# Performance work log

Measured on AMD Instinct MI355X. Metric: run time of the kernel, lower is better.

Reference implementation:

```python
import jax, jax.numpy as jnp
import numpy as np

N_RAYS = 8192
N_SAMPLES = 64
N_IMPORTANCE = 64
N_UP_ITERS = 4
NEAR, FAR = 0.5, 4.0
S_FINAL = 64.0


def sdf_net(pts, W1, b1, W2, b2, W3, b3):
    # pts: [..., 3] -> sdf [...]
    h = jax.nn.relu(pts @ W1 + b1)
    h = jax.nn.relu(h @ W2 + b2)
    return (h @ W3 + b3)[..., 0]


def radiance_net(pts, dirs, R1, r1, R2, r2):
    x = jnp.concatenate([pts, dirs], axis=-1)  # [..., 6]
    h = jax.nn.relu(x @ R1 + r1)
    return jax.nn.sigmoid(h @ R2 + r2)  # [..., 3]


def cdf_Phi_s(x, s):
    return jax.nn.sigmoid(x * s)


def alpha_to_w(alpha):
    # w_i = alpha_i * prod_{j<i} (1 - alpha_j)
    shifted = jnp.concatenate([jnp.ones_like(alpha[..., :1]), 1.0 - alpha + 1e-10], axis=-1)
    return alpha * jnp.cumprod(shifted, axis=-1)[..., :-1]


def sample_pdf(bins, weights, N):
    # bins: [R, M], weights: [R, M-1]; deterministic inverse-CDF sampling
    weights = weights + 1e-5
    pdf = weights / jnp.sum(weights, axis=-1, keepdims=True)
    cdf = jnp.cumsum(pdf, axis=-1)
    cdf = jnp.concatenate([jnp.zeros_like(cdf[..., :1]), cdf], axis=-1)  # [R, M]
    u = jnp.broadcast_to(jnp.linspace(0.0, 1.0, N, dtype=bins.dtype), cdf.shape[:-1] + (N,))
    inds = jax.vmap(lambda c, uu: jnp.searchsorted(c, uu, side='right'))(cdf, u)
    M = cdf.shape[-1]
    below = jnp.clip(inds - 1, 0, M - 1)
    above = jnp.clip(inds, 0, M - 1)
    cdf_b = jnp.take_along_axis(cdf, below, -1)
    cdf_a = jnp.take_along_axis(cdf, above, -1)
    bins_b = jnp.take_along_axis(bins, below, -1)
    bins_a = jnp.take_along_axis(bins, above, -1)
    denom = cdf_a - cdf_b
    denom = jnp.where(denom < 1e-5, jnp.ones_like(denom), denom)
    t = (u - cdf_b) / denom
    return bins_b + t * (bins_a - bins_b)


def _forward(rays_o, rays_d, W1, b1, W2, b2, W3, b3, R1, r1, R2, r2, s_val):
    rays_o = rays_o.reshape(-1, 3).astype(jnp.float32)
    rays_d = rays_d.reshape(-1, 3).astype(jnp.float32)
    rays_d = rays_d / jnp.linalg.norm(rays_d, axis=-1, keepdims=True)

    _t = jnp.linspace(0.0, 1.0, N_SAMPLES, dtype=jnp.float32)
    near = jnp.full((rays_o.shape[0], 1), NEAR, dtype=jnp.float32)
    far = jnp.full((rays_o.shape[0], 1), FAR, dtype=jnp.float32)
    d = near * (1.0 - _t) + far * _t  # [R, N_SAMPLES]

    sdf_fn = lambda p: sdf_net(p, W1, b1, W2, b2, W3, b3)

    # --- hierarchical upsampling (no_grad in original; stop_gradient at end) ---
    sdf = sdf_fn(rays_o[:, None, :] + d[..., None] * rays_d[:, None, :])
    for i in range(N_UP_ITERS):
        prev_sdf, next_sdf = sdf[..., :-1], sdf[..., 1:]
        prev_z, next_z = d[..., :-1], d[..., 1:]
        mid_sdf = 0.5 * (prev_sdf + next_sdf)
        dot_val = (next_sdf - prev_sdf) / (next_z - prev_z + 1e-5)
        prev_dot = jnp.concatenate([jnp.zeros_like(dot_val[..., :1]), dot_val[..., :-1]], axis=-1)
        dot_val = jnp.clip(jnp.minimum(prev_dot, dot_val), -10.0, 0.0)
        dist = next_z - prev_z
        prev_esti = mid_sdf - dot_val * dist * 0.5
        next_esti = mid_sdf + dot_val * dist * 0.5
        s_i = 64.0 * (2.0 ** i)
        prev_cdf = cdf_Phi_s(prev_esti, s_i)
        next_cdf = cdf_Phi_s(next_esti, s_i)
        alpha = (prev_cdf - next_cdf + 1e-5) / (prev_cdf + 1e-5)
        w = alpha_to_w(alpha)
        d_fine = sample_pdf(d, w, N_IMPORTANCE // N_UP_ITERS)
        d = jnp.concatenate([d, d_fine], axis=-1)
        sdf_fine = sdf_fn(rays_o[:, None, :] + d_fine[..., None] * rays_d[:, None, :])
        sdf = jnp.concatenate([sdf, sdf_fine], axis=-1)
        idx = jnp.argsort(d, axis=-1)
        d = jnp.take_along_axis(d, idx, axis=-1)
        sdf = jnp.take_along_axis(sdf, idx, axis=-1)
    d_all = jax.lax.stop_gradient(d)  # [R, 128]

    # --- final compositing ---
    pts = rays_o[:, None, :] + d_all[..., None] * rays_d[:, None, :]  # [R, 128, 3]
    d_mid = 0.5 * (d_all[..., 1:] + d_all[..., :-1])  # [R, 127]
    pts_mid = rays_o[:, None, :] + d_mid[..., None] * rays_d[:, None, :]

    sdf_final = sdf_fn(pts)  # [R, 128]
    s = s_val[0] * S_FINAL
    cdf = cdf_Phi_s(sdf_final, s)
    opacity_alpha = jnp.clip((cdf[..., :-1] - cdf[..., 1:] + 1e-5) / (cdf[..., :-1] + 1e-5), 0.0, 1.0)  # [R, 127]

    view_dirs = jnp.broadcast_to(rays_d[:, None, :], pts_mid.shape)
    radiances = radiance_net(pts_mid, view_dirs, R1, r1, R2, r2)  # [R, 127, 3]

    vis_w = alpha_to_w(opacity_alpha)  # [R, 127]
    rgb_map = jnp.sum(vis_w[..., None] * radiances, axis=-2)  # [R, 3]
    depth_map = jnp.sum(vis_w * d_mid, axis=-1)  # [R]
    acc_map = jnp.sum(vis_w, axis=-1)  # [R]
    return jnp.concatenate([rgb_map, depth_map[..., None], acc_map[..., None]], axis=-1)  # [R, 5]


def setup_inputs() -> dict:
    key = jax.random.key(0)
    ks = jax.random.split(key, 16)
    W = 128
    sc = 0.3
    return {
        'rays_o': jax.random.normal(ks[0], (N_RAYS, 3), jnp.float32),
        'rays_d': jax.random.normal(ks[1], (N_RAYS, 3), jnp.float32),
        'W1': sc * jax.random.normal(ks[2], (3, W), jnp.float32),
        'b1': sc * jax.random.normal(ks[3], (W,), jnp.float32),
        'W2': sc / np.sqrt(W) * jax.random.normal(ks[4], (W, W), jnp.float32),
        'b2': sc * jax.random.normal(ks[5], (W,), jnp.float32),
        'W3': sc / np.sqrt(W) * jax.random.normal(ks[6], (W, 1), jnp.float32),
        'b3': sc * jax.random.normal(ks[7], (1,), jnp.float32),
        'R1': sc * jax.random.normal(ks[8], (6, W), jnp.float32),
        'r1': sc * jax.random.normal(ks[9], (W,), jnp.float32),
        'R2': sc / np.sqrt(W) * jax.random.normal(ks[10], (W, 3), jnp.float32),
        'r2': sc * jax.random.normal(ks[11], (3,), jnp.float32),
        's_val': jnp.ones((1,), jnp.float32),
    }


def reference(rays_o, rays_d, W1, b1, W2, b2, W3, b3, R1, r1, R2, r2, s_val):
    return _forward(rays_o, rays_d, W1, b1, W2, b2, W3, b3, R1, r1, R2, r2, s_val)
```

## Files before the change

### kernel.cpp

```cpp
#include <hip/hip_runtime.h>
#include <math.h>

#define NRAYS 8192
#define RPB 8
#define AS 136

typedef _Float16 half8 __attribute__((ext_vector_type(8)));
typedef float floatx4 __attribute__((ext_vector_type(4)));

__device__ __forceinline__ float sigm(float x){ return 1.0f/(1.0f + __expf(-x)); }

__device__ __forceinline__ void wsync(){
  __builtin_amdgcn_wave_barrier();
  __builtin_amdgcn_s_waitcnt(0xc07f);
  __builtin_amdgcn_wave_barrier();
}

__launch_bounds__(512, 4)
__global__ void neus_render_kernel(
    const float* __restrict__ rays_o, const float* __restrict__ rays_d,
    const float* __restrict__ W1, const float* __restrict__ b1,
    const float* __restrict__ W2, const float* __restrict__ b2,
    const float* __restrict__ W3, const float* __restrict__ b3,
    const float* __restrict__ R1, const float* __restrict__ r1,
    const float* __restrict__ R2, const float* __restrict__ r2,
    const float* __restrict__ s_val, float* __restrict__ out)
{
  __shared__ __align__(16) _Float16 W2f[2048*8];
  __shared__ __align__(16) _Float16 R2f[256*8];
  __shared__ __align__(16) _Float16 Ah[RPB][16*AS];
  __shared__ __align__(16) float sDm[RPB][128];
  __shared__ __align__(16) float sSm[RPB][128];
  __shared__ __align__(16) float fDs[RPB][16];
  __shared__ __align__(16) float fSs[RPB][16];
  __shared__ float b2f[128], w3f[128];

  const int t = threadIdx.x;

  #pragma unroll
  for (int r=0;r<4;r++){
    int row = t + r*512;
    int i = row>>8, kt=(row>>6)&3, lr=row&63;
    int q = lr>>4, n = i*16 + (lr&15);
    half8 v;
    #pragma unroll
    for (int j=0;j<8;j++) v[j] = (_Float16)W2[(kt*32+q*8+j)*128 + n];
    *(half8*)&W2f[row*8] = v;
  }
  if (t < 256){
    int kt=t>>6, lr=t&63, q=lr>>4, col=lr&15;
    half8 v;
    #pragma unroll
    for (int j=0;j<8;j++){
      int k = kt*32+q*8+j;
      v[j] = (col<3) ? (_Float16)R2[k*3+col] : (_Float16)0.0f;
    }
    *(half8*)&R2f[t*8] = v;
  }
  if (t < 128){ b2f[t]=b2[t]; w3f[t]=W3[t]; }
  __syncthreads();

  const int wv = t>>6, l = t&63, l15 = t&15, q4 = (t>>4)&3;
  const int ray = blockIdx.x*RPB + wv;

  float ro0 = rays_o[ray*3+0], ro1 = rays_o[ray*3+1], ro2 = rays_o[ray*3+2];
  float rx  = rays_d[ray*3+0], ry  = rays_d[ray*3+1], rz  = rays_d[ray*3+2];
  float nrm = sqrtf(rx*rx + ry*ry + rz*rz);
  float rd0 = rx/nrm, rd1 = ry/nrm, rd2 = rz/nrm;
  float sfin = s_val[0] * 64.0f;
  float b3v = b3[0];
  float r2lane = (l15==0) ? r2[0] : (l15==1) ? r2[1] : (l15==2) ? r2[2] : 0.0f;

  float u10, v10, u11, v11, uR0, vR0, uR1, vR1;
  {
    int k=l;
    float a=W1[k], b=W1[128+k], c=W1[256+k];
    u10 = rd0*a+rd1*b+rd2*c; v10 = ro0*a+ro1*b+ro2*c + b1[k];
    float p=R1[k], qq=R1[128+k], s=R1[256+k], d=R1[384+k], e=R1[512+k], f=R1[640+k];
    uR0 = rd0*p+rd1*qq+rd2*s;
    vR0 = ro0*p+ro1*qq+ro2*s + rd0*d+rd1*e+rd2*f + r1[k];
  }
  {
    int k=64+l;
    float a=W1[k], b=W1[128+k], c=W1[256+k];
    u11 = rd0*a+rd1*b+rd2*c; v11 = ro0*a+ro1*b+ro2*c + b1[k];
    float p=R1[k], qq=R1[128+k], s=R1[256+k], d=R1[384+k], e=R1[512+k], f=R1[640+k];
    uR1 = rd0*p+rd1*qq+rd2*s;
    vR1 = ro0*p+ro1*qq+ro2*s + rd0*d+rd1*e+rd2*f + r1[k];
  }

  _Float16* Ahw = &Ah[wv][0];
  float* sD = &sDm[wv][0];
  float* sS = &sSm[wv][0];

  auto eval16 = [&](const float* dptr, float* dstptr){
    const float4* dp4 = (const float4*)dptr;
    float4 dva = dp4[0], dvb = dp4[1], dvc = dp4[2], dvd = dp4[3];
    float dvals[16] = {dva.x,dva.y,dva.z,dva.w, dvb.x,dvb.y,dvb.z,dvb.w,
                       dvc.x,dvc.y,dvc.z,dvc.w, dvd.x,dvd.y,dvd.z,dvd.w};
    #pragma unroll
    for (int m=0;m<16;m++){
      float h0 = fmaxf(fmaf(dvals[m], u10, v10), 0.0f);
      float h1 = fmaxf(fmaf(dvals[m], u11, v11), 0.0f);
      Ahw[m*AS + l]      = (_Float16)h0;
      Ahw[m*AS + 64 + l] = (_Float16)h1;
    }
    wsync();
    half8 A[4];
    #pragma unroll
    for (int kt=0;kt<4;kt++)
      A[kt] = *(const half8*)&Ahw[l15*AS + kt*32 + q4*8];
    floatx4 acc[8];
    #pragma unroll
    for (int i=0;i<8;i++) acc[i] = (floatx4){0.f,0.f,0.f,0.f};
    #pragma unroll
    for (int i=0;i<8;i++){
      #pragma unroll
      for (int kt=0;kt<4;kt++){
        half8 B = *(const half8*)&W2f[((i*4+kt)*64 + l)*8];
        acc[i] = __builtin_amdgcn_mfma_f32_16x16x32_f16(A[kt], B, acc[i], 0,0,0);
      }
    }
    float p0=0.f,p1=0.f,p2=0.f,p3=0.f;
    #pragma unroll
    for (int i=0;i<8;i++){
      float bb = b2f[i*16+l15], ww = w3f[i*16+l15];
      p0 += fmaxf(acc[i][0]+bb,0.0f)*ww;
      p1 += fmaxf(acc[i][1]+bb,0.0f)*ww;
      p2 += fmaxf(acc[i][2]+bb,0.0f)*ww;
      p3 += fmaxf(acc[i][3]+bb,0.0f)*ww;
    }
    #pragma unroll
    for (int off=1; off<16; off<<=1){
      p0 += __shfl_xor(p0, off, 64);
      p1 += __shfl_xor(p1, off, 64);
      p2 += __shfl_xor(p2, off, 64);
      p3 += __shfl_xor(p3, off, 64);
    }
    if (l15==0){
      floatx4 o = {p0+b3v, p1+b3v, p2+b3v, p3+b3v};
      *((floatx4*)&dstptr[q4*4]) = o;
    }
    wsync();
  };

  {
    float tt = (float)l / 63.0f;
    sD[l] = 0.5f*(1.0f-tt) + 4.0f*tt;
  }
  wsync();
  for (int c=0;c<4;c++) eval16(&sD[c*16], &sS[c*16]);

  for (int it=0; it<4; it++){
    const int n = 64 + 16*it;
    const int m = n-1;
    const float s_i = 64.0f * (float)(1<<it);

    float dc0 = sD[l],  sc0 = sS[l];
    float dn0 = sD[l+1], snn0 = sS[l+1];
    int lp0 = (l==0)?0:(l-1);
    float dp0 = sD[lp0], sp0 = sS[lp0];
    int i1 = 64+l;
    float dc1 = sD[i1 & 127], sc1 = sS[i1 & 127];
    int i1n = (i1+1) & 127;
    float dn1 = sD[i1n], snn1 = sS[i1n];
    float dp1 = sD[(i1-1) & 127], sp1 = sS[(i1-1) & 127];

    auto alpha_at = [&](float dp, float dc, float dn, float sp, float sc, float sn,
                        bool hasprev)->float{
      float mid = 0.5f*(sc+sn);
      float dv = (sn-sc)/(dn-dc+1e-5f);
      float pdv = hasprev ? (sc-sp)/(dc-dp+1e-5f) : 0.0f;
      float d2 = fminf(fminf(pdv,dv), 0.0f); d2 = fmaxf(d2,-10.0f);
      float dist = dn-dc;
      float pe = mid - d2*dist*0.5f, ne = mid + d2*dist*0.5f;
      float pc = sigm(pe*s_i), nc = sigm(ne*s_i);
      return (pc-nc+1e-5f)/(pc+1e-5f);
    };
    bool va0 = (l < m), va1 = (i1 < m);
    float a0 = va0 ? alpha_at(dp0,dc0,dn0,sp0,sc0,snn0, l>0)  : 0.0f;
    float a1 = va1 ? alpha_at(dp1,dc1,dn1,sp1,sc1,snn1, true) : 0.0f;

    float g0 = va0 ? (1.0f-a0+1e-10f) : 1.0f;
    float g1 = va1 ? (1.0f-a1+1e-10f) : 1.0f;
    #pragma unroll
    for (int off=1; off<64; off<<=1){ float y=__shfl_up(g0,off,64); if (l>=off) g0*=y; }
    float gtot0 = __shfl(g0, 63, 64);
    #pragma unroll
    for (int off=1; off<64; off<<=1){ float y=__shfl_up(g1,off,64); if (l>=off) g1*=y; }
    g1 *= gtot0;
    float T0 = __shfl_up(g0, 1, 64); if (l==0) T0 = 1.0f;
    float T1 = __shfl_up(g1, 1, 64); if (l==0) T1 = gtot0;

    float w0 = va0 ? (a0*T0 + 1e-5f) : 0.0f;
    float w1 = va1 ? (a1*T1 + 1e-5f) : 0.0f;
    #pragma unroll
    for (int off=1; off<64; off<<=1){ float y=__shfl_up(w0,off,64); if (l>=off) w0+=y; }
    float wtot0 = __shfl(w0, 63, 64);
    #pragma unroll
    for (int off=1; off<64; off<<=1){ float y=__shfl_up(w1,off,64); if (l>=off) w1+=y; }
    w1 += wtot0;
    float S = (m-1 < 64) ? __shfl(w0, m-1, 64) : __shfl(w1, m-65, 64);

    float csp0 = __shfl_up(w0, 1, 64);
    float cdf0 = (l==0) ? 0.0f : csp0/S;
    float csp1 = __shfl_up(w1, 1, 64);
    float c63  = __shfl(w0, 63, 64);
    float cdf1r = ((l==0) ? c63 : csp1)/S;
    float cdf1m = (i1 < n) ? cdf1r : 2.0f;

    int ind = 0;
    #pragma unroll
    for (int q=0;q<16;q++){
      float u = (float)q/15.0f;
      unsigned long long bq0 = __ballot(cdf0 <= u);
      unsigned long long bq1 = __ballot(cdf1m <= u);
      int c = __popcll(bq0) + __popcll(bq1);
      if (l==q) ind = c;
    }
    {
      float u = (float)l15/15.0f;
      int below = ind-1; if (below<0) below=0; if (below>n-1) below=n-1;
      int above = ind;   if (above>n-1) above=n-1;
      float cb = (below<64) ? __shfl(cdf0, below, 64) : __shfl(cdf1r, below-64, 64);
      float ca = (above<64) ? __shfl(cdf0, above, 64) : __shfl(cdf1r, above-64, 64);
      float bb = sD[below], ba = sD[above];
      float den = ca - cb; if (den < 1e-5f) den = 1.0f;
      float tt = (u - cb)/den;
      float fdnew = bb + tt*(ba-bb);
      if (l < 16) fDs[wv][l] = fdnew;
    }
    wsync();

    eval16(&fDs[wv][0], &fSs[wv][0]);

    {
      const float4* fp4 = (const float4*)&fDs[wv][0];
      float4 fa = fp4[0], fb = fp4[1], fc = fp4[2], fd = fp4[3];
      float fq[16] = {fa.x,fa.y,fa.z,fa.w, fb.x,fb.y,fb.z,fb.w,
                      fc.x,fc.y,fc.z,fc.w, fd.x,fd.y,fd.z,fd.w};
      float fdv = fDs[wv][l15];
      float fsv = fSs[wv][l15];
      bool v1 = (i1 < n);
      int rold0 = l, rold1 = i1;
      #pragma unroll
      for (int q=0;q<16;q++){
        rold0 += (fq[q] < dc0) ? 1 : 0;
        rold1 += (fq[q] < dc1) ? 1 : 0;
      }
      int rf = 0;
      #pragma unroll
      for (int q=0;q<16;q++){
        unsigned long long bq0 = __ballot(dc0 <= fq[q]);
        unsigned long long bq1 = __ballot(v1 && (dc1 <= fq[q]));
        int c = q + __popcll(bq0) + __popcll(bq1);
        if (l==q) rf = c;
      }
      wsync();
      sD[rold0] = dc0; sS[rold0] = sc0;
      if (v1){ sD[rold1] = dc1; sS[rold1] = sc1; }
      if (l < 16){ sD[rf] = fdv; sS[rf] = fsv; }
      wsync();
    }
  }

  float dm0, dm1, vw0, vw1;
  {
    float d0 = sD[l],  d1 = sD[64+l];
    float s0 = sS[l],  s1 = sS[64+l];
    float dn0 = sD[l+1], sn0 = sS[l+1];
    int i1n = (65+l) & 127;
    float dn1 = sD[i1n], sn1 = sS[i1n];
    bool v1a = (l < 63);
    float cf0 = sigm(s0*sfin), cfn0 = sigm(sn0*sfin);
    float a0 = (cf0-cfn0+1e-5f)/(cf0+1e-5f);
    a0 = fminf(fmaxf(a0,0.0f),1.0f);
    float cf1 = sigm(s1*sfin), cfn1 = sigm(sn1*sfin);
    float a1 = (cf1-cfn1+1e-5f)/(cf1+1e-5f);
    a1 = v1a ? fminf(fmaxf(a1,0.0f),1.0f) : 0.0f;
    dm0 = 0.5f*(d0+dn0);
    dm1 = v1a ? 0.5f*(d1+dn1) : 0.0f;

    float g0 = 1.0f-a0+1e-10f;
    float g1 = v1a ? (1.0f-a1+1e-10f) : 1.0f;
    #pragma unroll
    for (int off=1; off<64; off<<=1){ float y=__shfl_up(g0,off,64); if (l>=off) g0*=y; }
    float gtot0 = __shfl(g0, 63, 64);
    #pragma unroll
    for (int off=1; off<64; off<<=1){ float y=__shfl_up(g1,off,64); if (l>=off) g1*=y; }
    g1 *= gtot0;
    float T0 = __shfl_up(g0, 1, 64); if (l==0) T0 = 1.0f;
    float T1 = __shfl_up(g1, 1, 64); if (l==0) T1 = gtot0;
    vw0 = a0*T0;
    vw1 = a1*T1;
    wsync();
    sD[l] = dm0; sD[64+l] = dm1;
    sS[l] = vw0; sS[64+l] = vw1;
    wsync();
  }

  half8 RB[4];
  #pragma unroll
  for (int kt=0;kt<4;kt++) RB[kt] = *(const half8*)&R2f[(kt*64+l)*8];
  float rgb = 0.0f;
  for (int g=0; g<8; g++){
    const float4* dp4 = (const float4*)&sDm[wv][g*16];
    float4 dva = dp4[0], dvb = dp4[1], dvc = dp4[2], dvd = dp4[3];
    float dvals[16] = {dva.x,dva.y,dva.z,dva.w, dvb.x,dvb.y,dvb.z,dvb.w,
                       dvc.x,dvc.y,dvc.z,dvc.w, dvd.x,dvd.y,dvd.z,dvd.w};
    #pragma unroll
    for (int m=0;m<16;m++){
      float h0 = fmaxf(fmaf(dvals[m], uR0, vR0), 0.0f);
      float h1 = fmaxf(fmaf(dvals[m], uR1, vR1), 0.0f);
      Ahw[m*AS + l]      = (_Float16)h0;
      Ahw[m*AS + 64 + l] = (_Float16)h1;
    }
    wsync();
    half8 A[4];
    #pragma unroll
    for (int kt=0;kt<4;kt++)
      A[kt] = *(const half8*)&Ahw[l15*AS + kt*32 + q4*8];
    floatx4 racc = (floatx4){0.f,0.f,0.f,0.f};
    #pragma unroll
    for (int kt=0;kt<4;kt++)
      racc = __builtin_amdgcn_mfma_f32_16x16x32_f16(A[kt], RB[kt], racc, 0,0,0);
    #pragma unroll
    for (int r=0;r<4;r++){
      int pt = g*16 + q4*4 + r;
      float w = sS[pt];
      rgb += w * sigm(racc[r] + r2lane);
    }
    wsync();
  }

  float v3 = dm0*vw0 + dm1*vw1;
  float v4 = vw0 + vw1;
  #pragma unroll
  for (int off=32; off>=1; off>>=1){
    v3 += __shfl_xor(v3, off, 64);
    v4 += __shfl_xor(v4, off, 64);
  }
  rgb += __shfl_xor(rgb, 16, 64);
  rgb += __shfl_xor(rgb, 32, 64);
  if (l < 3)  out[ray*5 + l] = rgb;
  if (l == 3) out[ray*5 + 3] = v3;
  if (l == 4) out[ray*5 + 4] = v4;
}

extern "C" void kernel_launch(void* const* d_in, const int* in_sizes, int n_in,
                              void* d_out, int out_size, void* d_ws, size_t ws_size,
                              hipStream_t stream) {
  const float* rays_o = (const float*)d_in[0];
  const float* rays_d = (const float*)d_in[1];
  const float* W1 = (const float*)d_in[2];
  const float* b1 = (const float*)d_in[3];
  const float* W2 = (const float*)d_in[4];
  const float* b2 = (const float*)d_in[5];
  const float* W3 = (const float*)d_in[6];
  const float* b3 = (const float*)d_in[7];
  const float* R1 = (const float*)d_in[8];
  const float* r1 = (const float*)d_in[9];
  const float* R2 = (const float*)d_in[10];
  const float* r2 = (const float*)d_in[11];
  const float* sv = (const float*)d_in[12];
  float* out = (float*)d_out;
  neus_render_kernel<<<NRAYS/RPB, 512, 0, stream>>>(
      rays_o, rays_d, W1, b1, W2, b2, W3, b3, R1, r1, R2, r2, sv, out);
}
```

Baseline: 188.5 us.

## Split SDF hidden activations into fp16 hi/lo pairs for extra MFMA precision

```diff
diff --git a/kernel.cpp b/kernel.cpp
--- a/kernel.cpp
+++ b/kernel.cpp
@@ -6,6 +6,7 @@
 #define AS 136
 
 typedef _Float16 half8 __attribute__((ext_vector_type(8)));
+typedef _Float16 half2v __attribute__((ext_vector_type(2)));
 typedef float floatx4 __attribute__((ext_vector_type(4)));
 
 __device__ __forceinline__ float sigm(float x){ return 1.0f/(1.0f + __expf(-x)); }
@@ -15,6 +16,82 @@
   __builtin_amdgcn_s_waitcnt(0xc07f);
   __builtin_amdgcn_wave_barrier();
 }
+
+#define EVAL16(dptr_, dstptr_) do { \
+  const float* dp_ = (dptr_); \
+  _Pragma("unroll") \
+  for (int mq=0;mq<4;mq++){ \
+    float4 dv4 = ((const float4*)dp_)[mq]; \
+    float h0_, h1_; \
+    h0_ = fmaxf(fmaf(dv4.x, u10, v10), 0.0f); h1_ = fmaxf(fmaf(dv4.x, u11, v11), 0.0f); \
+    *(half2v*)&Ahw[(mq*4+0)*AS + 2*l] = (half2v){(_Float16)h0_, (_Float16)h1_}; \
+    h0_ = fmaxf(fmaf(dv4.y, u10, v10), 0.0f); h1_ = fmaxf(fmaf(dv4.y, u11, v11), 0.0f); \
+    *(half2v*)&Ahw[(mq*4+1)*AS + 2*l] = (half2v){(_Float16)h0_, (_Float16)h1_}; \
+    h0_ = fmaxf(fmaf(dv4.z, u10, v10), 0.0f); h1_ = fmaxf(fmaf(dv4.z, u11, v11), 0.0f); \
+    *(half2v*)&Ahw[(mq*4+2)*AS + 2*l] = (half2v){(_Float16)h0_, (_Float16)h1_}; \
+    h0_ = fmaxf(fmaf(dv4.w, u10, v10), 0.0f); h1_ = fmaxf(fmaf(dv4.w, u11, v11), 0.0f); \
+    *(half2v*)&Ahw[(mq*4+3)*AS + 2*l] = (half2v){(_Float16)h0_, (_Float16)h1_}; \
+  } \
+  wsync(); \
+  half8 Ahi0 = *(const half8*)&Ahw[l15*AS +   0 + q4*8]; \
+  half8 Ahi1 = *(const half8*)&Ahw[l15*AS +  32 + q4*8]; \
+  half8 Ahi2 = *(const half8*)&Ahw[l15*AS +  64 + q4*8]; \
+  half8 Ahi3 = *(const half8*)&Ahw[l15*AS +  96 + q4*8]; \
+  wsync();    \
+  _Pragma("unroll") \
+  for (int mq=0;mq<4;mq++){ \
+    float4 dv4 = ((const float4*)dp_)[mq]; \
+    float h0_, h1_; _Float16 hh0_, hh1_; \
+    h0_ = fmaxf(fmaf(dv4.x, u10, v10), 0.0f); h1_ = fmaxf(fmaf(dv4.x, u11, v11), 0.0f); \
+    hh0_=(_Float16)h0_; hh1_=(_Float16)h1_; \
+    *(half2v*)&Ahw[(mq*4+0)*AS + 2*l] = (half2v){(_Float16)(h0_-(float)hh0_), (_Float16)(h1_-(float)hh1_)}; \
+    h0_ = fmaxf(fmaf(dv4.y, u10, v10), 0.0f); h1_ = fmaxf(fmaf(dv4.y, u11, v11), 0.0f); \
+    hh0_=(_Float16)h0_; hh1_=(_Float16)h1_; \
+    *(half2v*)&Ahw[(mq*4+1)*AS + 2*l] = (half2v){(_Float16)(h0_-(float)hh0_), (_Float16)(h1_-(float)hh1_)}; \
+    h0_ = fmaxf(fmaf(dv4.z, u10, v10), 0.0f); h1_ = fmaxf(fmaf(dv4.z, u11, v11), 0.0f); \
+    hh0_=(_Float16)h0_; hh1_=(_Float16)h1_; \
+    *(half2v*)&Ahw[(mq*4+2)*AS + 2*l] = (half2v){(_Float16)(h0_-(float)hh0_), (_Float16)(h1_-(float)hh1_)}; \
+    h0_ = fmaxf(fmaf(dv4.w, u10, v10), 0.0f); h1_ = fmaxf(fmaf(dv4.w, u11, v11), 0.0f); \
+    hh0_=(_Float16)h0_; hh1_=(_Float16)h1_; \
+    *(half2v*)&Ahw[(mq*4+3)*AS + 2*l] = (half2v){(_Float16)(h0_-(float)hh0_), (_Float16)(h1_-(float)hh1_)}; \
+  } \
+  wsync(); \
+  floatx4 acc[8]; \
+  _Pragma("unroll") \
+  for (int i=0;i<8;i++) acc[i] = (floatx4){0.f,0.f,0.f,0.f}; \
+  _Pragma("unroll") \
+  for (int kt=0;kt<4;kt++){ \
+    half8 Ahi_ = (kt==0)?Ahi0:(kt==1)?Ahi1:(kt==2)?Ahi2:Ahi3; \
+    half8 Alo_ = *(const half8*)&Ahw[l15*AS + kt*32 + q4*8]; \
+    _Pragma("unroll") \
+    for (int i=0;i<8;i++){ \
+      half8 B_ = *(const half8*)&W2f[((i*4+kt)*64 + l)*8]; \
+      acc[i] = __builtin_amdgcn_mfma_f32_16x16x32_f16(Ahi_, B_, acc[i], 0,0,0); \
+      acc[i] = __builtin_amdgcn_mfma_f32_16x16x32_f16(Alo_, B_, acc[i], 0,0,0); \
+    } \
+  } \
+  float p0=0.f,p1=0.f,p2=0.f,p3=0.f; \
+  _Pragma("unroll") \
+  for (int i=0;i<8;i++){ \
+    float bb = b2f[i*16+l15], ww = w3f[i*16+l15]; \
+    p0 += fmaxf(acc[i][0]+bb,0.0f)*ww; \
+    p1 += fmaxf(acc[i][1]+bb,0.0f)*ww; \
+    p2 += fmaxf(acc[i][2]+bb,0.0f)*ww; \
+    p3 += fmaxf(acc[i][3]+bb,0.0f)*ww; \
+  } \
+  _Pragma("unroll") \
+  for (int off=1; off<16; off<<=1){ \
+    p0 += __shfl_xor(p0, off, 64); \
+    p1 += __shfl_xor(p1, off, 64); \
+    p2 += __shfl_xor(p2, off, 64); \
+    p3 += __shfl_xor(p3, off, 64); \
+  } \
+  if (l15==0){ \
+    floatx4 o_ = {p0+b3v, p1+b3v, p2+b3v, p3+b3v}; \
+    *((floatx4*)&(dstptr_)[q4*4]) = o_; \
+  } \
+  wsync(); \
+} while(0)
 
 __launch_bounds__(512, 4)
 __global__ void neus_render_kernel(
@@ -62,94 +139,32 @@
 
   const int wv = t>>6, l = t&63, l15 = t&15, q4 = (t>>4)&3;
   const int ray = blockIdx.x*RPB + wv;
-
-  float ro0 = rays_o[ray*3+0], ro1 = rays_o[ray*3+1], ro2 = rays_o[ray*3+2];
-  float rx  = rays_d[ray*3+0], ry  = rays_d[ray*3+1], rz  = rays_d[ray*3+2];
-  float nrm = sqrtf(rx*rx + ry*ry + rz*rz);
-  float rd0 = rx/nrm, rd1 = ry/nrm, rd2 = rz/nrm;
-  float sfin = s_val[0] * 64.0f;
   float b3v = b3[0];
-  float r2lane = (l15==0) ? r2[0] : (l15==1) ? r2[1] : (l15==2) ? r2[2] : 0.0f;
-
-  float u10, v10, u11, v11, uR0, vR0, uR1, vR1;
+
+  float u10, v10, u11, v11;
   {
-    int k=l;
+    float ro0 = rays_o[ray*3+0], ro1 = rays_o[ray*3+1], ro2 = rays_o[ray*3+2];
+    float rx  = rays_d[ray*3+0], ry  = rays_d[ray*3+1], rz  = rays_d[ray*3+2];
+    float nrm = sqrtf(rx*rx + ry*ry + rz*rz);
+    float rd0 = rx/nrm, rd1 = ry/nrm, rd2 = rz/nrm;
+    int k=2*l;
     float a=W1[k], b=W1[128+k], c=W1[256+k];
     u10 = rd0*a+rd1*b+rd2*c; v10 = ro0*a+ro1*b+ro2*c + b1[k];
-    float p=R1[k], qq=R1[128+k], s=R1[256+k], d=R1[384+k], e=R1[512+k], f=R1[640+k];
-    uR0 = rd0*p+rd1*qq+rd2*s;
-    vR0 = ro0*p+ro1*qq+ro2*s + rd0*d+rd1*e+rd2*f + r1[k];
-  }
-  {
-    int k=64+l;
-    float a=W1[k], b=W1[128+k], c=W1[256+k];
+    k=2*l+1;
+    a=W1[k]; b=W1[128+k]; c=W1[256+k];
     u11 = rd0*a+rd1*b+rd2*c; v11 = ro0*a+ro1*b+ro2*c + b1[k];
-    float p=R1[k], qq=R1[128+k], s=R1[256+k], d=R1[384+k], e=R1[512+k], f=R1[640+k];
-    uR1 = rd0*p+rd1*qq+rd2*s;
-    vR1 = ro0*p+ro1*qq+ro2*s + rd0*d+rd1*e+rd2*f + r1[k];
   }
 
   _Float16* Ahw = &Ah[wv][0];
   float* sD = &sDm[wv][0];
   float* sS = &sSm[wv][0];
 
-  auto eval16 = [&](const float* dptr, float* dstptr){
-    const float4* dp4 = (const float4*)dptr;
-    float4 dva = dp4[0], dvb = dp4[1], dvc = dp4[2], dvd = dp4[3];
-    float dvals[16] = {dva.x,dva.y,dva.z,dva.w, dvb.x,dvb.y,dvb.z,dvb.w,
-                       dvc.x,dvc.y,dvc.z,dvc.w, dvd.x,dvd.y,dvd.z,dvd.w};
-    #pragma unroll
-    for (int m=0;m<16;m++){
-      float h0 = fmaxf(fmaf(dvals[m], u10, v10), 0.0f);
-      float h1 = fmaxf(fmaf(dvals[m], u11, v11), 0.0f);
-      Ahw[m*AS + l]      = (_Float16)h0;
-      Ahw[m*AS + 64 + l] = (_Float16)h1;
-    }
-    wsync();
-    half8 A[4];
-    #pragma unroll
-    for (int kt=0;kt<4;kt++)
-      A[kt] = *(const half8*)&Ahw[l15*AS + kt*32 + q4*8];
-    floatx4 acc[8];
-    #pragma unroll
-    for (int i=0;i<8;i++) acc[i] = (floatx4){0.f,0.f,0.f,0.f};
-    #pragma unroll
-    for (int i=0;i<8;i++){
-      #pragma unroll
-      for (int kt=0;kt<4;kt++){
-        half8 B = *(const half8*)&W2f[((i*4+kt)*64 + l)*8];
-        acc[i] = __builtin_amdgcn_mfma_f32_16x16x32_f16(A[kt], B, acc[i], 0,0,0);
-      }
-    }
-    float p0=0.f,p1=0.f,p2=0.f,p3=0.f;
-    #pragma unroll
-    for (int i=0;i<8;i++){
-      float bb = b2f[i*16+l15], ww = w3f[i*16+l15];
-      p0 += fmaxf(acc[i][0]+bb,0.0f)*ww;
-      p1 += fmaxf(acc[i][1]+bb,0.0f)*ww;
-      p2 += fmaxf(acc[i][2]+bb,0.0f)*ww;
-      p3 += fmaxf(acc[i][3]+bb,0.0f)*ww;
-    }
-    #pragma unroll
-    for (int off=1; off<16; off<<=1){
-      p0 += __shfl_xor(p0, off, 64);
-      p1 += __shfl_xor(p1, off, 64);
-      p2 += __shfl_xor(p2, off, 64);
-      p3 += __shfl_xor(p3, off, 64);
-    }
-    if (l15==0){
-      floatx4 o = {p0+b3v, p1+b3v, p2+b3v, p3+b3v};
-      *((floatx4*)&dstptr[q4*4]) = o;
-    }
-    wsync();
-  };
-
   {
     float tt = (float)l / 63.0f;
     sD[l] = 0.5f*(1.0f-tt) + 4.0f*tt;
   }
   wsync();
-  for (int c=0;c<4;c++) eval16(&sD[c*16], &sS[c*16]);
+  for (int c=0;c<4;c++) EVAL16(&sD[c*16], &sS[c*16]);
 
   for (int it=0; it<4; it++){
     const int n = 64 + 16*it;
@@ -232,7 +247,7 @@
     }
     wsync();
 
-    eval16(&fDs[wv][0], &fSs[wv][0]);
+    EVAL16(&fDs[wv][0], &fSs[wv][0]);
 
     {
       const float4* fp4 = (const float4*)&fDs[wv][0];
@@ -266,6 +281,7 @@
 
   float dm0, dm1, vw0, vw1;
   {
+    float sfin = s_val[0] * 64.0f;
     float d0 = sD[l],  d1 = sD[64+l];
     float s0 = sS[l],  s1 = sS[64+l];
     float dn0 = sD[l+1], sn0 = sS[l+1];
@@ -299,21 +315,40 @@
     wsync();
   }
 
+  float uR0, vR0, uR1, vR1, r2lane;
+  {
+    float ro0 = rays_o[ray*3+0], ro1 = rays_o[ray*3+1], ro2 = rays_o[ray*3+2];
+    float rx  = rays_d[ray*3+0], ry  = rays_d[ray*3+1], rz  = rays_d[ray*3+2];
+    float nrm = sqrtf(rx*rx + ry*ry + rz*rz);
+    float rd0 = rx/nrm, rd1 = ry/nrm, rd2 = rz/nrm;
+    int k=2*l;
+    float p=R1[k], qq=R1[128+k], s=R1[256+k], d=R1[384+k], e=R1[512+k], f=R1[640+k];
+    uR0 = rd0*p+rd1*qq+rd2*s;
+    vR0 = ro0*p+ro1*qq+ro2*s + rd0*d+rd1*e+rd2*f + r1[k];
+    k=2*l+1;
+    p=R1[k]; qq=R1[128+k]; s=R1[256+k]; d=R1[384+k]; e=R1[512+k]; f=R1[640+k];
+    uR1 = rd0*p+rd1*qq+rd2*s;
+    vR1 = ro0*p+ro1*qq+ro2*s + rd0*d+rd1*e+rd2*f + r1[k];
+    r2lane = (l15==0) ? r2[0] : (l15==1) ? r2[1] : (l15==2) ? r2[2] : 0.0f;
+  }
+
   half8 RB[4];
   #pragma unroll
   for (int kt=0;kt<4;kt++) RB[kt] = *(const half8*)&R2f[(kt*64+l)*8];
   float rgb = 0.0f;
   for (int g=0; g<8; g++){
-    const float4* dp4 = (const float4*)&sDm[wv][g*16];
-    float4 dva = dp4[0], dvb = dp4[1], dvc = dp4[2], dvd = dp4[3];
-    float dvals[16] = {dva.x,dva.y,dva.z,dva.w, dvb.x,dvb.y,dvb.z,dvb.w,
-                       dvc.x,dvc.y,dvc.z,dvc.w, dvd.x,dvd.y,dvd.z,dvd.w};
-    #pragma unroll
-    for (int m=0;m<16;m++){
-      float h0 = fmaxf(fmaf(dvals[m], uR0, vR0), 0.0f);
-      float h1 = fmaxf(fmaf(dvals[m], uR1, vR1), 0.0f);
-      Ahw[m*AS + l]      = (_Float16)h0;
-      Ahw[m*AS + 64 + l] = (_Float16)h1;
+    #pragma unroll
+    for (int mq=0;mq<4;mq++){
+      float4 dv4 = ((const float4*)&sDm[wv][g*16])[mq];
+      float h0, h1;
+      h0 = fmaxf(fmaf(dv4.x, uR0, vR0), 0.0f); h1 = fmaxf(fmaf(dv4.x, uR1, vR1), 0.0f);
+      *(half2v*)&Ahw[(mq*4+0)*AS + 2*l] = (half2v){(_Float16)h0, (_Float16)h1};
+      h0 = fmaxf(fmaf(dv4.y, uR0, vR0), 0.0f); h1 = fmaxf(fmaf(dv4.y, uR1, vR1), 0.0f);
+      *(half2v*)&Ahw[(mq*4+1)*AS + 2*l] = (half2v){(_Float16)h0, (_Float16)h1};
+      h0 = fmaxf(fmaf(dv4.z, uR0, vR0), 0.0f); h1 = fmaxf(fmaf(dv4.z, uR1, vR1), 0.0f);
+      *(half2v*)&Ahw[(mq*4+2)*AS + 2*l] = (half2v){(_Float16)h0, (_Float16)h1};
+      h0 = fmaxf(fmaf(dv4.w, uR0, vR0), 0.0f); h1 = fmaxf(fmaf(dv4.w, uR1, vR1), 0.0f);
+      *(half2v*)&Ahw[(mq*4+3)*AS + 2*l] = (half2v){(_Float16)h0, (_Float16)h1};
     }
     wsync();
     half8 A[4];
```

After: 202.8 us. 1.08x slower.
